# Optimization experiments

Hardware: AMD Instinct MI355X
Metric: run time of the kernel (lower is better)

## Reference

```python
import jax, jax.numpy as jnp
import numpy as np

NUM_ITER = 4
MIN_DISP = 1.0 / 100.0  # 1/max_depth
MAX_DISP = 1.0 / 0.1    # 1/min_depth


def _diag_embed(v):
    return v[..., :, None] * jnp.eye(v.shape[-1], dtype=v.dtype)


def _v2m(r):  # r: [B,3,1] -> antisymmetric [B,3,3]
    a1, a2, a3 = r[:, 0, 0], r[:, 1, 0], r[:, 2, 0]
    z = jnp.zeros_like(a1)
    return jnp.stack([z, -a3, a2, a3, z, -a1, -a2, a1, z], axis=-1).reshape(-1, 3, 3)


def _se3_pose(se3):  # se3: [B,6,1] -> [B,3,4]
    B = se3.shape[0]
    t, w = se3[:, 0:3], se3[:, 3:6]
    Nr = jnp.maximum(jnp.sqrt(jnp.sum(w * w, axis=1, keepdims=True)), 1e-12)  # [B,1,1]
    r = w / Nr
    I = jnp.eye(3, dtype=se3.dtype)[None]
    rx = _v2m(r)
    c, s = jnp.cos(Nr), jnp.sin(Nr)
    R = c * I + (1.0 - c) * jnp.matmul(r, jnp.transpose(r, (0, 2, 1))) + s * rx
    J = I + (Nr - s) / Nr * jnp.matmul(rx, rx) + (1.0 - c) / Nr * rx
    T = jnp.matmul(J, t)
    return jnp.concatenate([R, T], axis=2)


def _homogeneous(p34):
    B = p34.shape[0]
    ext = jnp.broadcast_to(jnp.array([[[0.0, 0.0, 0.0, 1.0]]], dtype=p34.dtype), (B, 1, 4))
    return jnp.concatenate([p34, ext], axis=1)


def _project_2d3d(points, depth, K_inv):  # [B,2,N],[B,1,N] -> [B,3,N]
    ones = jnp.ones_like(points[:, :1])
    xy3d = jnp.concatenate([points, ones], axis=1)
    return jnp.matmul(K_inv, xy3d) * depth


def _project_3d2d(p3d, K):
    q = jnp.matmul(K, p3d)
    return q[:, 0:2] / jnp.maximum(q[:, 2:3], 0.01)


def _reproject_error(p1, p2, disp, pose, K, K_inv):
    depth = 1.0 / jnp.maximum(disp, 0.01)
    p3d = _project_2d3d(p1, depth, K_inv)
    p3d_hat = jnp.matmul(pose[:, :3, :3], p3d) + pose[:, :3, 3:]
    return p2 - _project_3d2d(p3d_hat, K)


def _mean_on_mask(data, mask):  # reduce over last (point) dim, keepdims
    return jnp.sum(data * mask, axis=2, keepdims=True) / jnp.sum(mask, axis=2, keepdims=True)


def _jacobi_pose(p3d, K):  # -> [B,2,6,N]
    B, _, N = p3d.shape
    fx, fy = K[:, 0:1, 0:1], K[:, 1:2, 1:2]
    X, Y = p3d[:, 0:1], p3d[:, 1:2]
    Z = jnp.maximum(p3d[:, 2:3], 1e-12)
    iZ = 1.0 / Z
    iZ2 = iZ * iZ
    z = jnp.zeros_like(X)
    rows = [fx * iZ, z, -fx * X * iZ2, -fx * X * Y * iZ2, fx + fx * X * X * iZ2, -fx * Y * iZ,
            z, fy * iZ, -fy * Y * iZ2, -fy - fy * Y * Y * iZ2, fy * X * Y * iZ2, fy * X * iZ]
    return -jnp.concatenate(rows, axis=1).reshape(B, 2, 6, N)


def _jacobi_disp(p3d, pose, disps):  # -> [B,2,1,N]
    B, _, N = p3d.shape
    fx, fy = K0 = pose  # placeholder avoided below
    raise NotImplementedError


def _jacobi_disp_impl(p3d, pose, K, disps):  # -> [B,2,1,N]
    B, _, N = p3d.shape
    fx, fy = K[:, 0:1, 0:1], K[:, 1:2, 1:2]
    X, Y = p3d[:, 0:1], p3d[:, 1:2]
    Z = jnp.maximum(p3d[:, 2:3], 1e-12)
    iZ = 1.0 / Z
    iZ2 = iZ * iZ
    z = jnp.zeros_like(X)
    J1 = jnp.concatenate([fx * iZ, z, -fx * X * iZ2, z, fy * iZ, -fy * Y * iZ2], axis=1)
    J1 = jnp.transpose(J1.reshape(B, 2, 3, N), (0, 3, 1, 2))  # [B,N,2,3]
    T = pose[:, :3, 3:]  # [B,3,1]
    DD = -1.0 / disps    # [B,1,N]
    J2 = jnp.concatenate([DD * (X - T[:, 0:1]), (Y - T[:, 1:2]) * DD, (Z - T[:, 2:3]) * DD], axis=1)
    J2 = jnp.transpose(J2.reshape(B, 3, 1, N), (0, 3, 1, 2))  # [B,N,3,1]
    J = -jnp.matmul(J1, J2)                                   # [B,N,2,1]
    return jnp.transpose(J, (0, 2, 3, 1))                     # [B,2,1,N]


def _huber_w(err, mask, b=9.0):  # diag values of the [B,N,2,2] weight -> [B,N,2]
    B, _, N = err.shape
    en = jnp.sqrt(jnp.sum(err * err, axis=1, keepdims=True))          # [B,1,N]
    w = jnp.minimum(b / jnp.maximum(en, 1e-12), 1.0)
    w = jnp.sqrt(w) * mask                                            # [B,1,N]
    w = jnp.broadcast_to(jnp.transpose(w, (0, 2, 1)), (B, N, 2))
    return jax.lax.stop_gradient(w)


def _marginalization(Bm, E, C, V, W, L):
    Bsz, N = E.shape[0], E.shape[1]
    Bm = Bm + _diag_embed(jnp.diagonal(Bm, axis1=-2, axis2=-1)) * L   # L:[B,1,1]
    C = C + C * L.reshape(Bsz, 1, 1, 1)                               # C diag is itself (1x1)
    C_inv = 1.0 / jnp.maximum(C, 1.0)
    Bm = Bm + jnp.eye(6, dtype=Bm.dtype)
    Ev = E[..., 0]                 # [B,N,6]
    cinv = C_inv[:, :, 0, 0]       # [B,N]
    Wv = W[:, :, 0, 0]             # [B,N]
    Hsc = jnp.einsum('bn,bni,bnj->bij', cinv, Ev, Ev) / N
    bsc = (jnp.einsum('bn,bni,bn->bi', cinv, Ev, Wv) / N)[..., None]  # [B,6,1]
    invL = 1.0 / (1.0 + L)
    left = Bm - Hsc * invL
    right = V - bsc * invL
    s = 1.0 / jnp.sqrt(jnp.diagonal(left, axis1=-2, axis2=-1) + 10.0)  # [B,6]
    D = _diag_embed(s)
    H = D @ left @ D
    delta_pose = D @ jnp.linalg.solve(H, D @ right)                   # [B,6,1]
    p3d_sc = jnp.einsum('bni,bi->bn', Ev, delta_pose[:, :, 0]) * invL[:, 0, 0][:, None]
    delta_points = cinv * (Wv - p3d_sc)                               # [B,N]
    return delta_pose, delta_points


def _lm_step(pts_coord, pts_disp, pose, K, K_inv, mask, L):
    B, _, N = pts_coord.shape
    pts_depth = 1.0 / pts_disp
    p3d = _project_2d3d(pts_coord[:, 0:2], pts_depth, K_inv)
    p3d_hat = jnp.matmul(pose[:, :3, :3], p3d) + pose[:, :3, 3:]
    p2d_hat = _project_3d2d(p3d_hat, K)
    errors = pts_coord[:, 2:4] - p2d_hat                     # [B,2,N]
    J_pose = _jacobi_pose(p3d_hat, K)                        # [B,2,6,N]
    J_disp = _jacobi_disp_impl(p3d_hat, pose, K, pts_disp)   # [B,2,1,N]
    w = _huber_w(errors, mask)                               # [B,N,2]
    w2 = w * w
    Jp_T = jnp.transpose(J_pose, (0, 3, 2, 1))               # [B,N,6,2]
    Jd_T = jnp.transpose(J_disp, (0, 3, 2, 1))               # [B,N,1,2]
    Jp = jnp.transpose(J_pose, (0, 3, 1, 2))                 # [B,N,2,6]
    Jd = jnp.transpose(J_disp, (0, 3, 1, 2))                 # [B,N,2,1]
    Bm = jnp.einsum('bnik,bnkj->bij', Jp_T * w2[:, :, None, :], Jp) / N
    E = jnp.matmul(Jp_T * w2[:, :, None, :], Jd)             # [B,N,6,1]
    C = jnp.matmul(Jd_T * w2[:, :, None, :], Jd)             # [B,N,1,1]
    e = jnp.transpose(errors, (0, 2, 1))[..., None]          # [B,N,2,1]
    g_pose = -jnp.einsum('bnik,bnkj->bij', Jp_T * w[:, :, None, :], e) / N  # [B,6,1]
    g_disp = -jnp.matmul(Jd_T * w[:, :, None, :], e)         # [B,N,1,1]
    delta_pose, delta_points = _marginalization(Bm, E, C, g_pose, g_disp, L)
    return delta_pose, delta_points[:, None, :]              # [B,6,1], [B,1,N]


def reference(pts_coord, pts_disp, pose, K, K_inv, mask, L):
    for _ in range(NUM_ITER):
        dp, dd = _lm_step(pts_coord, pts_disp, pose, K, K_inv, mask, L)
        disp_new = jnp.clip(pts_disp + dd, MIN_DISP, MAX_DISP)
        pose_new = jnp.matmul(_homogeneous(_se3_pose(dp)), pose)
        e1 = _reproject_error(pts_coord[:, 0:2], pts_coord[:, 2:4], disp_new, pose_new, K, K_inv)
        e2 = _reproject_error(pts_coord[:, 0:2], pts_coord[:, 2:4], pts_disp, pose, K, K_inv)
        r1 = _mean_on_mask(jnp.linalg.norm(e1, axis=1, keepdims=True), mask)
        r2 = _mean_on_mask(jnp.linalg.norm(e2, axis=1, keepdims=True), mask)
        M = jax.lax.stop_gradient((r1 < r2).astype(pose.dtype))  # [B,1,1]
        pts_disp = jnp.where(M == 1, disp_new, pts_disp)
        pose = jnp.where(M == 1, pose_new, pose)
        L = jnp.clip(jnp.where(M == 1, L * 0.5, L * 5.0), 0.01, 1e6)
    return pose, pts_disp


def setup_inputs() -> dict:
    B, N = 8, 131072
    W, H = 640, 480
    key = jax.random.key(0)
    k = jax.random.split(key, 4)
    p1 = jax.random.uniform(k[0], (B, 2, N), dtype=jnp.float32) * jnp.array([W, H], jnp.float32).reshape(1, 2, 1)
    p2 = p1 + jax.random.normal(k[1], (B, 2, N), dtype=jnp.float32) * 2.0
    pts_coord = jnp.concatenate([p1, p2], axis=1)                      # [B,4,N]
    pts_disp = jax.random.uniform(k[2], (B, 1, N), dtype=jnp.float32, minval=0.05, maxval=2.0)
    pose = jnp.tile(jnp.eye(4, dtype=jnp.float32)[None], (B, 1, 1))
    pose = pose.at[:, :3, 3].set(jax.random.normal(k[3], (B, 3), dtype=jnp.float32) * 0.05)
    K = jnp.tile(jnp.array([[320.0, 0.0, 320.0], [0.0, 320.0, 240.0], [0.0, 0.0, 1.0]], jnp.float32)[None], (B, 1, 1))
    K_inv = jnp.linalg.inv(K)
    mask = jnp.ones((B, 1, N), jnp.float32)
    L = jnp.ones((B, 1, 1), jnp.float32) * 0.01
    return {'pts_coord': pts_coord, 'pts_disp': pts_disp, 'pose': pose, 'K': K, 'K_inv': K_inv, 'mask': mask, 'L': L}
```

## Files before the change

### kernel.cpp

```cpp
#include <hip/hip_runtime.h>
#include <math.h>


constexpr int TPB  = 256;
constexpr int BLKA = 64;
constexpr int NRED = 54;

__device__ __forceinline__ float wave_red(float v) {
#pragma unroll
  for (int m = 32; m; m >>= 1) v += __shfl_xor(v, m, 64);
  return v;
}

__device__ __forceinline__ float reproj_norm(
    float x1, float y1, float x2, float y2, float d,
    const float* P, const float* Kc, const float* Ki) {
  float depth = 1.0f / fmaxf(d, 0.01f);
  float pxx = (Ki[0]*x1 + Ki[1]*y1 + Ki[2]) * depth;
  float pyy = (Ki[3]*x1 + Ki[4]*y1 + Ki[5]) * depth;
  float pzz = (Ki[6]*x1 + Ki[7]*y1 + Ki[8]) * depth;
  float X = P[0]*pxx + P[1]*pyy + P[2]*pzz + P[3];
  float Y = P[4]*pxx + P[5]*pyy + P[6]*pzz + P[7];
  float Z = P[8]*pxx + P[9]*pyy + P[10]*pzz + P[11];
  float q0 = Kc[0]*X + Kc[1]*Y + Kc[2]*Z;
  float q1 = Kc[3]*X + Kc[4]*Y + Kc[5]*Z;
  float q2 = Kc[6]*X + Kc[7]*Y + Kc[8]*Z;
  float iZc = 1.0f / fmaxf(q2, 0.01f);
  float ex = x2 - q0*iZc, ey = y2 - q1*iZc;
  return sqrtf(ex*ex + ey*ey);
}

__device__ __forceinline__ float accept_M(const float* __restrict__ partB,
                                          int b) {
  float r1 = 0.0f, r2 = 0.0f, ms = 0.0f;
  for (int j = 0; j < BLKA; j++) {
    const float* p = partB + ((size_t)b*BLKA + j)*3;
    r1 += p[0]; r2 += p[1]; ms += p[2];
  }
  return ((r1/ms) < (r2/ms)) ? 1.0f : 0.0f;
}

__global__ __launch_bounds__(TPB) void kA(
    int it,
    const float* __restrict__ pts, const float* __restrict__ disp_src,
    const float* __restrict__ prop, const float* __restrict__ mask,
    const float* __restrict__ Kin, const float* __restrict__ Kiin,
    float* __restrict__ disp_cur,
    const float* __restrict__ pose0, const float* __restrict__ L0,
    const float* __restrict__ partB, const float* __restrict__ pose_new_ws,
    float* __restrict__ pose_slot_w, const float* __restrict__ pose_slot_r,
    float* __restrict__ L_slot_w, const float* __restrict__ L_slot_r,
    float* __restrict__ partA, int N) {
  const int b = blockIdx.y;

  __shared__ float sP[16];
  __shared__ float sMeta[2];
  if (threadIdx.x == 0) {
    float P[16], Lv, fs;
    if (it == 0) {
      for (int i = 0; i < 16; i++) P[i] = pose0[b*16+i];
      Lv = L0[b]; fs = 0.0f;
    } else {
      float M = accept_M(partB, b);
      fs = M;
      float Lp = L_slot_r[b];
      float Ln = (M != 0.0f) ? Lp*0.5f : Lp*5.0f;
      Lv = fminf(fmaxf(Ln, 0.01f), 1000000.0f);
      for (int i = 0; i < 16; i++)
        P[i] = (M != 0.0f) ? pose_new_ws[b*16+i] : pose_slot_r[b*16+i];
    }
    for (int i = 0; i < 16; i++) sP[i] = P[i];
    sMeta[0] = fs; sMeta[1] = Lv;
    if (blockIdx.x == 0) {
      for (int i = 0; i < 16; i++) pose_slot_w[b*16+i] = P[i];
      L_slot_w[b] = Lv;
    }
  }
  __syncthreads();

  float Kc[9], Ki[9], P[12];
#pragma unroll
  for (int i = 0; i < 9; i++) { Kc[i] = Kin[b*9+i]; Ki[i] = Kiin[b*9+i]; }
#pragma unroll
  for (int i = 0; i < 12; i++) P[i] = sP[i];
  const float onepL = 1.0f + sMeta[1];
  const float fsel = sMeta[0];
  const float fx = Kc[0], fy = Kc[4];

  float acc[NRED];
#pragma unroll
  for (int k = 0; k < NRED; k++) acc[k] = 0.0f;

  const size_t bN = (size_t)b * N;
  const float* px1 = pts + (size_t)b*4*N;
  const float* py1 = px1 + N;
  const float* px2 = px1 + 2*(size_t)N;
  const float* py2 = px1 + 3*(size_t)N;

  for (int n = blockIdx.x*TPB + threadIdx.x; n < N; n += gridDim.x*TPB) {
    float x1 = px1[n], y1 = py1[n], x2 = px2[n], y2 = py2[n];
    float d = disp_src[bN+n];
    if (fsel != 0.0f) d = prop[bN+n];
    disp_cur[bN+n] = d;
    float m = mask[bN+n];

    float depth = 1.0f / d;
    float pxx = (Ki[0]*x1 + Ki[1]*y1 + Ki[2]) * depth;
    float pyy = (Ki[3]*x1 + Ki[4]*y1 + Ki[5]) * depth;
    float pzz = (Ki[6]*x1 + Ki[7]*y1 + Ki[8]) * depth;
    float X = P[0]*pxx + P[1]*pyy + P[2]*pzz + P[3];
    float Y = P[4]*pxx + P[5]*pyy + P[6]*pzz + P[7];
    float Z = P[8]*pxx + P[9]*pyy + P[10]*pzz + P[11];
    float q0 = Kc[0]*X + Kc[1]*Y + Kc[2]*Z;
    float q1 = Kc[3]*X + Kc[4]*Y + Kc[5]*Z;
    float q2 = Kc[6]*X + Kc[7]*Y + Kc[8]*Z;
    float iZc = 1.0f / fmaxf(q2, 0.01f);
    float ex = x2 - q0*iZc;
    float ey = y2 - q1*iZc;
    float iZ = 1.0f / fmaxf(Z, 1e-12f);
    float iZ2 = iZ*iZ;

    float jp0[6], jp1[6];
    jp0[0] = -(fx*iZ);  jp0[1] = 0.0f;       jp0[2] = fx*X*iZ2;
    jp0[3] = fx*X*Y*iZ2; jp0[4] = -(fx + fx*X*X*iZ2); jp0[5] = fx*Y*iZ;
    jp1[0] = 0.0f;      jp1[1] = -(fy*iZ);   jp1[2] = fy*Y*iZ2;
    jp1[3] = fy + fy*Y*Y*iZ2; jp1[4] = -(fy*X*Y*iZ2); jp1[5] = -(fy*X*iZ);

    float DD = -depth;
    float dx = X - P[3], dy = Y - P[7], dz = Z - P[11];
    float jd0 = -((fx*iZ)*(DD*dx) - (fx*X*iZ2)*(DD*dz));
    float jd1 = -((fy*iZ)*(DD*dy) - (fy*Y*iZ2)*(DD*dz));

    float en = sqrtf(ex*ex + ey*ey);
    float wmin = fminf(9.0f / fmaxf(en, 1e-12f), 1.0f);
    float w  = sqrtf(wmin) * m;
    float w2 = w * w;

    float E[6];
#pragma unroll
    for (int k = 0; k < 6; k++) E[k] = w2*(jp0[k]*jd0 + jp1[k]*jd1);
    float C = w2*(jd0*jd0 + jd1*jd1);
    float cinv = 1.0f / fmaxf(C*onepL, 1.0f);
    float Wv = -w*(jd0*ex + jd1*ey);

    int idx = 0;
#pragma unroll
    for (int k = 0; k < 6; k++)
#pragma unroll
      for (int l = k; l < 6; l++) { acc[idx] += w2*(jp0[k]*jp0[l] + jp1[k]*jp1[l]); idx++; }
#pragma unroll
    for (int k = 0; k < 6; k++) acc[21+k] -= w*(jp0[k]*ex + jp1[k]*ey);
    idx = 27;
#pragma unroll
    for (int k = 0; k < 6; k++)
#pragma unroll
      for (int l = k; l < 6; l++) { acc[idx] += (cinv*E[k])*E[l]; idx++; }
#pragma unroll
    for (int k = 0; k < 6; k++) acc[48+k] += cinv*E[k]*Wv;
  }

  __shared__ float lds[TPB/64][NRED];
  const int lane = threadIdx.x & 63, wvi = threadIdx.x >> 6;
#pragma unroll
  for (int k = 0; k < NRED; k++) {
    float v = wave_red(acc[k]);
    if (lane == 0) lds[wvi][k] = v;
  }
  __syncthreads();
  if (threadIdx.x < NRED) {
    float s = 0.0f;
#pragma unroll
    for (int wq = 0; wq < TPB/64; wq++) s += lds[wq][threadIdx.x];
    partA[((size_t)b*gridDim.x + blockIdx.x)*NRED + threadIdx.x] = s;
  }
}

__global__ __launch_bounds__(TPB) void kB(
    const float* __restrict__ pts, const float* __restrict__ disp_cur,
    const float* __restrict__ mask,
    const float* __restrict__ Kin, const float* __restrict__ Kiin,
    const float* __restrict__ pose_slot, const float* __restrict__ L_slot,
    const float* __restrict__ partA,
    float* __restrict__ pose_new_ws,
    float* __restrict__ prop, float* __restrict__ partB, int N) {
  const int b = blockIdx.y;
  const float L = L_slot[b];

  __shared__ float S[NRED];
  __shared__ float sPn[16];
  __shared__ float sdp[6];
  if (threadIdx.x < NRED) {
    float s = 0.0f;
    for (int j = 0; j < BLKA; j++)
      s += partA[((size_t)b*BLKA + j)*NRED + threadIdx.x];
    S[threadIdx.x] = s;
  }
  __syncthreads();
  if (threadIdx.x == 0) {
    const float invN = 1.0f / (float)N;
    float Bm[6][6], Hs[6][6], g[6], bs[6];
    {
      int idx = 0;
      for (int k = 0; k < 6; k++)
        for (int l = k; l < 6; l++) { float v = S[idx++]*invN; Bm[k][l] = v; Bm[l][k] = v; }
      for (int k = 0; k < 6; k++) g[k] = S[21+k]*invN;
      idx = 27;
      for (int k = 0; k < 6; k++)
        for (int l = k; l < 6; l++) { float v = S[idx++]*invN; Hs[k][l] = v; Hs[l][k] = v; }
      for (int k = 0; k < 6; k++) bs[k] = S[48+k]*invN;
    }
    const float invL = 1.0f / (1.0f + L);
    float left[6][6], right[6];
    for (int k = 0; k < 6; k++) {
      for (int l = 0; l < 6; l++) {
        float v = Bm[k][l] - Hs[k][l]*invL;
        if (k == l) v += Bm[k][k]*L + 1.0f;
        left[k][l] = v;
      }
      right[k] = g[k] - bs[k]*invL;
    }
    float sv[6];
    for (int k = 0; k < 6; k++) sv[k] = 1.0f / sqrtf(left[k][k] + 10.0f);
    float H[6][7];
    for (int k = 0; k < 6; k++) {
      for (int l = 0; l < 6; l++) H[k][l] = sv[k]*left[k][l]*sv[l];
      H[k][6] = sv[k]*right[k];
    }
    for (int c = 0; c < 6; c++) {
      int piv = c; float mx = fabsf(H[c][c]);
      for (int r = c+1; r < 6; r++) { float a = fabsf(H[r][c]); if (a > mx) { mx = a; piv = r; } }
      if (piv != c)
        for (int cc2 = c; cc2 < 7; cc2++) { float tmp = H[c][cc2]; H[c][cc2] = H[piv][cc2]; H[piv][cc2] = tmp; }
      float ip = 1.0f / H[c][c];
      for (int r = c+1; r < 6; r++) {
        float f = H[r][c]*ip;
        for (int cc2 = c; cc2 < 7; cc2++) H[r][cc2] -= f*H[c][cc2];
      }
    }
    float x[6];
    for (int c = 5; c >= 0; c--) {
      float v = H[c][6];
      for (int cc2 = c+1; cc2 < 6; cc2++) v -= H[c][cc2]*x[cc2];
      x[c] = v / H[c][c];
    }
    float dp[6];
    for (int k = 0; k < 6; k++) { dp[k] = sv[k]*x[k]; sdp[k] = dp[k]; }

    float tx = dp[0], ty = dp[1], tz = dp[2];
    float wx = dp[3], wy = dp[4], wz = dp[5];
    float Nr = fmaxf(sqrtf(wx*wx + wy*wy + wz*wz), 1e-12f);
    float rx = wx/Nr, ry = wy/Nr, rz = wz/Nr;
    float c_ = cosf(Nr), sn = sinf(Nr);
    float omc = 1.0f - c_;
    float SK[3][3] = {{0.0f,-rz,ry},{rz,0.0f,-rx},{-ry,rx,0.0f}};
    float SK2[3][3];
    for (int i = 0; i < 3; i++)
      for (int j = 0; j < 3; j++) {
        float s2 = 0.0f;
        for (int k = 0; k < 3; k++) s2 += SK[i][k]*SK[k][j];
        SK2[i][j] = s2;
      }
    float rr[3] = {rx, ry, rz};
    float a = (Nr - sn)/Nr, bcoef = omc/Nr;
    float R3[3][3], Jm[3][3];
    for (int i = 0; i < 3; i++)
      for (int j = 0; j < 3; j++) {
        float eye = (i == j) ? 1.0f : 0.0f;
        R3[i][j] = c_*eye + omc*rr[i]*rr[j] + sn*SK[i][j];
        Jm[i][j] = eye + a*SK2[i][j] + bcoef*SK[i][j];
      }
    float T3[3];
    for (int i = 0; i < 3; i++) T3[i] = Jm[i][0]*tx + Jm[i][1]*ty + Jm[i][2]*tz;
    float Pc[16];
    for (int i = 0; i < 16; i++) Pc[i] = pose_slot[b*16+i];
    float Pn[16];
    for (int i = 0; i < 3; i++)
      for (int j = 0; j < 4; j++)
        Pn[i*4+j] = R3[i][0]*Pc[j] + R3[i][1]*Pc[4+j] + R3[i][2]*Pc[8+j] + T3[i]*Pc[12+j];
    for (int j = 0; j < 4; j++) Pn[12+j] = Pc[12+j];
    for (int i = 0; i < 16; i++) sPn[i] = Pn[i];
    if (blockIdx.x == 0)
      for (int i = 0; i < 16; i++) pose_new_ws[b*16+i] = Pn[i];
  }
  __syncthreads();

  float Kc[9], Ki[9], P[12], Pn[12], dp[6];
#pragma unroll
  for (int i = 0; i < 9; i++) { Kc[i] = Kin[b*9+i]; Ki[i] = Kiin[b*9+i]; }
#pragma unroll
  for (int i = 0; i < 12; i++) { P[i] = pose_slot[b*16+i]; Pn[i] = sPn[i]; }
#pragma unroll
  for (int i = 0; i < 6; i++) dp[i] = sdp[i];
  const float onepL = 1.0f + L;
  const float invL = 1.0f / onepL;
  const float fx = Kc[0], fy = Kc[4];

  float r1a = 0.0f, r2a = 0.0f, msa = 0.0f;
  const size_t bN = (size_t)b * N;
  const float* px1 = pts + (size_t)b*4*N;
  const float* py1 = px1 + N;
  const float* px2 = px1 + 2*(size_t)N;
  const float* py2 = px1 + 3*(size_t)N;

  for (int n = blockIdx.x*TPB + threadIdx.x; n < N; n += gridDim.x*TPB) {
    float x1 = px1[n], y1 = py1[n], x2 = px2[n], y2 = py2[n];
    float d = disp_cur[bN+n];
    float m = mask[bN+n];

    float depth = 1.0f / d;
    float pxx = (Ki[0]*x1 + Ki[1]*y1 + Ki[2]) * depth;
    float pyy = (Ki[3]*x1 + Ki[4]*y1 + Ki[5]) * depth;
    float pzz = (Ki[6]*x1 + Ki[7]*y1 + Ki[8]) * depth;
    float X = P[0]*pxx + P[1]*pyy + P[2]*pzz + P[3];
    float Y = P[4]*pxx + P[5]*pyy + P[6]*pzz + P[7];
    float Z = P[8]*pxx + P[9]*pyy + P[10]*pzz + P[11];
    float q0 = Kc[0]*X + Kc[1]*Y + Kc[2]*Z;
    float q1 = Kc[3]*X + Kc[4]*Y + Kc[5]*Z;
    float q2 = Kc[6]*X + Kc[7]*Y + Kc[8]*Z;
    float iZc = 1.0f / fmaxf(q2, 0.01f);
    float ex = x2 - q0*iZc;
    float ey = y2 - q1*iZc;
    float iZ = 1.0f / fmaxf(Z, 1e-12f);
    float iZ2 = iZ*iZ;

    float jp0[6], jp1[6];
    jp0[0] = -(fx*iZ);  jp0[1] = 0.0f;       jp0[2] = fx*X*iZ2;
    jp0[3] = fx*X*Y*iZ2; jp0[4] = -(fx + fx*X*X*iZ2); jp0[5] = fx*Y*iZ;
    jp1[0] = 0.0f;      jp1[1] = -(fy*iZ);   jp1[2] = fy*Y*iZ2;
    jp1[3] = fy + fy*Y*Y*iZ2; jp1[4] = -(fy*X*Y*iZ2); jp1[5] = -(fy*X*iZ);

    float DD = -depth;
    float dx = X - P[3], dy = Y - P[7], dz = Z - P[11];
    float jd0 = -((fx*iZ)*(DD*dx) - (fx*X*iZ2)*(DD*dz));
    float jd1 = -((fy*iZ)*(DD*dy) - (fy*Y*iZ2)*(DD*dz));

    float en = sqrtf(ex*ex + ey*ey);
    float wmin = fminf(9.0f / fmaxf(en, 1e-12f), 1.0f);
    float w  = sqrtf(wmin) * m;
    float w2 = w * w;

    float dotE = 0.0f;
#pragma unroll
    for (int k = 0; k < 6; k++) {
      float Ek = w2*(jp0[k]*jd0 + jp1[k]*jd1);
      dotE += Ek * dp[k];
    }
    float C = w2*(jd0*jd0 + jd1*jd1);
    float cinv = 1.0f / fmaxf(C*onepL, 1.0f);
    float Wv = -w*(jd0*ex + jd1*ey);

    float dnew = d + cinv*(Wv - dotE*invL);
    dnew = fminf(fmaxf(dnew, 0.01f), 10.0f);
    prop[bN+n] = dnew;

    float n1 = reproj_norm(x1, y1, x2, y2, dnew, Pn, Kc, Ki);
    float n2 = reproj_norm(x1, y1, x2, y2, d,    P,  Kc, Ki);
    r1a += n1*m; r2a += n2*m; msa += m;
  }

  __shared__ float lds[TPB/64][3];
  const int lane = threadIdx.x & 63, wvi = threadIdx.x >> 6;
  float v0 = wave_red(r1a), v1 = wave_red(r2a), v2 = wave_red(msa);
  if (lane == 0) { lds[wvi][0] = v0; lds[wvi][1] = v1; lds[wvi][2] = v2; }
  __syncthreads();
  if (threadIdx.x < 3) {
    float s = 0.0f;
#pragma unroll
    for (int wq = 0; wq < TPB/64; wq++) s += lds[wq][threadIdx.x];
    partB[((size_t)b*gridDim.x + blockIdx.x)*3 + threadIdx.x] = s;
  }
}

__global__ __launch_bounds__(TPB) void kF(
    const float* __restrict__ partB,
    const float* __restrict__ pose_slot, const float* __restrict__ pose_new_ws,
    const float* __restrict__ prop, float* __restrict__ dout, int N, int B) {
  const int b = blockIdx.y;
  __shared__ float sM[1];
  if (threadIdx.x == 0) sM[0] = accept_M(partB, b);
  __syncthreads();
  const float M = sM[0];

  if (blockIdx.x == 0 && threadIdx.x < 16) {
    float v = (M != 0.0f) ? pose_new_ws[b*16+threadIdx.x] : pose_slot[b*16+threadIdx.x];
    dout[b*16 + threadIdx.x] = v;
  }
  if (M == 0.0f) return;
  float* dd = dout + B*16;
  const size_t bN = (size_t)b * N;
  for (int n = blockIdx.x*TPB + threadIdx.x; n < N; n += gridDim.x*TPB)
    dd[bN+n] = prop[bN+n];
}

extern "C" void kernel_launch(void* const* d_in, const int* in_sizes, int n_in,
                              void* d_out, int out_size, void* d_ws, size_t ws_size,
                              hipStream_t stream) {
  const float* pts   = (const float*)d_in[0];
  const float* disp0 = (const float*)d_in[1];
  const float* pose0 = (const float*)d_in[2];
  const float* Kin   = (const float*)d_in[3];
  const float* Kiin  = (const float*)d_in[4];
  const float* mask  = (const float*)d_in[5];
  const float* L0    = (const float*)d_in[6];

  const int B = in_sizes[6];
  const int N = in_sizes[1] / B;
  const size_t BN = (size_t)B * N;

  float* out      = (float*)d_out;
  float* disp_cur = out + B*16;

  float* ws        = (float*)d_ws;
  float* prop      = ws;
  float* partA     = prop + BN;
  float* partB     = partA + (size_t)B*BLKA*NRED;
  float* pose_slots= partB + (size_t)B*BLKA*3;
  float* pose_new  = pose_slots + (size_t)2*B*16;
  float* L_slots   = pose_new + (size_t)B*16;

  dim3 gridBig(BLKA, B), blk(TPB);
  for (int it = 0; it < 4; ++it) {
    float* ps_w = pose_slots + (size_t)(it & 1) * B * 16;
    const float* ps_r = pose_slots + (size_t)((it + 1) & 1) * B * 16;
    float* Ls_w = L_slots + (size_t)(it & 1) * B;
    const float* Ls_r = L_slots + (size_t)((it + 1) & 1) * B;

    kA<<<gridBig, blk, 0, stream>>>(it, pts, (it == 0) ? disp0 : disp_cur, prop,
                                    mask, Kin, Kiin, disp_cur, pose0, L0,
                                    partB, pose_new, ps_w, ps_r, Ls_w, Ls_r,
                                    partA, N);
    kB<<<gridBig, blk, 0, stream>>>(pts, disp_cur, mask, Kin, Kiin,
                                    ps_w, Ls_w, partA, pose_new,
                                    prop, partB, N);
  }
  kF<<<gridBig, blk, 0, stream>>>(partB, pose_slots + (size_t)1*B*16, pose_new,
                                  prop, out, N, B);
}
```

Before: 285.4 us.

## Fuse all LM iterations into one cooperative kernel with register-resident disparities

Replaces the nine-kernel sequence (kA/kB per iteration plus kF) with a single cooperative launch of 256 blocks of 512 threads. Grid-wide syncs separate the reduction and solve phases, and each thread keeps its 8 disparities and proposals in registers across iterations, so the per-iteration global disp/prop round trips and launch overheads go away. The trade-offs are grid.sync latency, reliance on all blocks being co-resident, and higher register pressure from 54 accumulators plus 16 per-thread disparity values. If the cooperative launch fails, it falls back to the old multi-kernel path.

```diff
diff --git a/kernel.cpp b/kernel.cpp
--- a/kernel.cpp
+++ b/kernel.cpp
@@ -1,10 +1,18 @@
 #include <hip/hip_runtime.h>
+#include <hip/hip_cooperative_groups.h>
 #include <math.h>
 
+namespace cg = cooperative_groups;
+
+
+constexpr int NRED = 54;
+
+constexpr int CT   = 512;
+constexpr int CBPB = 32;
+constexpr int CPPT = 8;
 
 constexpr int TPB  = 256;
 constexpr int BLKA = 64;
-constexpr int NRED = 54;
 
 __device__ __forceinline__ float wave_red(float v) {
 #pragma unroll
@@ -30,8 +38,374 @@
   return sqrtf(ex*ex + ey*ey);
 }
 
-__device__ __forceinline__ float accept_M(const float* __restrict__ partB,
-                                          int b) {
+__device__ __forceinline__ void pointA(
+    float x1, float y1, float x2, float y2, float m, float d,
+    const float* P, const float* Kc, const float* Ki,
+    float fx, float fy, float onepL, float* acc) {
+  float depth = 1.0f / d;
+  float pxx = (Ki[0]*x1 + Ki[1]*y1 + Ki[2]) * depth;
+  float pyy = (Ki[3]*x1 + Ki[4]*y1 + Ki[5]) * depth;
+  float pzz = (Ki[6]*x1 + Ki[7]*y1 + Ki[8]) * depth;
+  float X = P[0]*pxx + P[1]*pyy + P[2]*pzz + P[3];
+  float Y = P[4]*pxx + P[5]*pyy + P[6]*pzz + P[7];
+  float Z = P[8]*pxx + P[9]*pyy + P[10]*pzz + P[11];
+  float q0 = Kc[0]*X + Kc[1]*Y + Kc[2]*Z;
+  float q1 = Kc[3]*X + Kc[4]*Y + Kc[5]*Z;
+  float q2 = Kc[6]*X + Kc[7]*Y + Kc[8]*Z;
+  float iZc = 1.0f / fmaxf(q2, 0.01f);
+  float ex = x2 - q0*iZc;
+  float ey = y2 - q1*iZc;
+  float iZ = 1.0f / fmaxf(Z, 1e-12f);
+  float iZ2 = iZ*iZ;
+
+  float jp0[6], jp1[6];
+  jp0[0] = -(fx*iZ);  jp0[1] = 0.0f;       jp0[2] = fx*X*iZ2;
+  jp0[3] = fx*X*Y*iZ2; jp0[4] = -(fx + fx*X*X*iZ2); jp0[5] = fx*Y*iZ;
+  jp1[0] = 0.0f;      jp1[1] = -(fy*iZ);   jp1[2] = fy*Y*iZ2;
+  jp1[3] = fy + fy*Y*Y*iZ2; jp1[4] = -(fy*X*Y*iZ2); jp1[5] = -(fy*X*iZ);
+
+  float DD = -depth;
+  float dx = X - P[3], dy = Y - P[7], dz = Z - P[11];
+  float jd0 = -((fx*iZ)*(DD*dx) - (fx*X*iZ2)*(DD*dz));
+  float jd1 = -((fy*iZ)*(DD*dy) - (fy*Y*iZ2)*(DD*dz));
+
+  float en = sqrtf(ex*ex + ey*ey);
+  float wmin = fminf(9.0f / fmaxf(en, 1e-12f), 1.0f);
+  float w  = sqrtf(wmin) * m;
+  float w2 = w * w;
+
+  float E[6];
+#pragma unroll
+  for (int k = 0; k < 6; k++) E[k] = w2*(jp0[k]*jd0 + jp1[k]*jd1);
+  float C = w2*(jd0*jd0 + jd1*jd1);
+  float cinv = 1.0f / fmaxf(C*onepL, 1.0f);
+  float Wv = -w*(jd0*ex + jd1*ey);
+
+  int idx = 0;
+#pragma unroll
+  for (int k = 0; k < 6; k++)
+#pragma unroll
+    for (int l = k; l < 6; l++) { acc[idx] += w2*(jp0[k]*jp0[l] + jp1[k]*jp1[l]); idx++; }
+#pragma unroll
+  for (int k = 0; k < 6; k++) acc[21+k] -= w*(jp0[k]*ex + jp1[k]*ey);
+  idx = 27;
+#pragma unroll
+  for (int k = 0; k < 6; k++)
+#pragma unroll
+    for (int l = k; l < 6; l++) { acc[idx] += (cinv*E[k])*E[l]; idx++; }
+#pragma unroll
+  for (int k = 0; k < 6; k++) acc[48+k] += cinv*E[k]*Wv;
+}
+
+__device__ __forceinline__ float pointB(
+    float x1, float y1, float x2, float y2, float m, float d,
+    const float* P, const float* Pn, const float* dp,
+    const float* Kc, const float* Ki,
+    float fx, float fy, float onepL, float invL,
+    float& r1a, float& r2a, float& msa) {
+  float depth = 1.0f / d;
+  float pxx = (Ki[0]*x1 + Ki[1]*y1 + Ki[2]) * depth;
+  float pyy = (Ki[3]*x1 + Ki[4]*y1 + Ki[5]) * depth;
+  float pzz = (Ki[6]*x1 + Ki[7]*y1 + Ki[8]) * depth;
+  float X = P[0]*pxx + P[1]*pyy + P[2]*pzz + P[3];
+  float Y = P[4]*pxx + P[5]*pyy + P[6]*pzz + P[7];
+  float Z = P[8]*pxx + P[9]*pyy + P[10]*pzz + P[11];
+  float q0 = Kc[0]*X + Kc[1]*Y + Kc[2]*Z;
+  float q1 = Kc[3]*X + Kc[4]*Y + Kc[5]*Z;
+  float q2 = Kc[6]*X + Kc[7]*Y + Kc[8]*Z;
+  float iZc = 1.0f / fmaxf(q2, 0.01f);
+  float ex = x2 - q0*iZc;
+  float ey = y2 - q1*iZc;
+  float iZ = 1.0f / fmaxf(Z, 1e-12f);
+  float iZ2 = iZ*iZ;
+
+  float jp0[6], jp1[6];
+  jp0[0] = -(fx*iZ);  jp0[1] = 0.0f;       jp0[2] = fx*X*iZ2;
+  jp0[3] = fx*X*Y*iZ2; jp0[4] = -(fx + fx*X*X*iZ2); jp0[5] = fx*Y*iZ;
+  jp1[0] = 0.0f;      jp1[1] = -(fy*iZ);   jp1[2] = fy*Y*iZ2;
+  jp1[3] = fy + fy*Y*Y*iZ2; jp1[4] = -(fy*X*Y*iZ2); jp1[5] = -(fy*X*iZ);
+
+  float DD = -depth;
+  float dx = X - P[3], dy = Y - P[7], dz = Z - P[11];
+  float jd0 = -((fx*iZ)*(DD*dx) - (fx*X*iZ2)*(DD*dz));
+  float jd1 = -((fy*iZ)*(DD*dy) - (fy*Y*iZ2)*(DD*dz));
+
+  float en = sqrtf(ex*ex + ey*ey);
+  float wmin = fminf(9.0f / fmaxf(en, 1e-12f), 1.0f);
+  float w  = sqrtf(wmin) * m;
+  float w2 = w * w;
+
+  float dotE = 0.0f;
+#pragma unroll
+  for (int k = 0; k < 6; k++) {
+    float Ek = w2*(jp0[k]*jd0 + jp1[k]*jd1);
+    dotE += Ek * dp[k];
+  }
+  float C = w2*(jd0*jd0 + jd1*jd1);
+  float cinv = 1.0f / fmaxf(C*onepL, 1.0f);
+  float Wv = -w*(jd0*ex + jd1*ey);
+
+  float dnew = d + cinv*(Wv - dotE*invL);
+  dnew = fminf(fmaxf(dnew, 0.01f), 10.0f);
+
+  float n1 = reproj_norm(x1, y1, x2, y2, dnew, Pn, Kc, Ki);
+  float n2 = reproj_norm(x1, y1, x2, y2, d,    P,  Kc, Ki);
+  r1a += n1*m; r2a += n2*m; msa += m;
+  return dnew;
+}
+
+__device__ void solve_scalar(const float* S, float L, const float* Pc_in,
+                             float invN, float* dp_out, float* Pn_out) {
+  float Bm[6][6], Hs[6][6], g[6], bs[6];
+  {
+    int idx = 0;
+    for (int k = 0; k < 6; k++)
+      for (int l = k; l < 6; l++) { float v = S[idx++]*invN; Bm[k][l] = v; Bm[l][k] = v; }
+    for (int k = 0; k < 6; k++) g[k] = S[21+k]*invN;
+    idx = 27;
+    for (int k = 0; k < 6; k++)
+      for (int l = k; l < 6; l++) { float v = S[idx++]*invN; Hs[k][l] = v; Hs[l][k] = v; }
+    for (int k = 0; k < 6; k++) bs[k] = S[48+k]*invN;
+  }
+  const float invL = 1.0f / (1.0f + L);
+  float left[6][6], right[6];
+  for (int k = 0; k < 6; k++) {
+    for (int l = 0; l < 6; l++) {
+      float v = Bm[k][l] - Hs[k][l]*invL;
+      if (k == l) v += Bm[k][k]*L + 1.0f;
+      left[k][l] = v;
+    }
+    right[k] = g[k] - bs[k]*invL;
+  }
+  float sv[6];
+  for (int k = 0; k < 6; k++) sv[k] = 1.0f / sqrtf(left[k][k] + 10.0f);
+  float H[6][7];
+  for (int k = 0; k < 6; k++) {
+    for (int l = 0; l < 6; l++) H[k][l] = sv[k]*left[k][l]*sv[l];
+    H[k][6] = sv[k]*right[k];
+  }
+  for (int c = 0; c < 6; c++) {
+    int piv = c; float mx = fabsf(H[c][c]);
+    for (int r = c+1; r < 6; r++) { float a = fabsf(H[r][c]); if (a > mx) { mx = a; piv = r; } }
+    if (piv != c)
+      for (int cc2 = c; cc2 < 7; cc2++) { float tmp = H[c][cc2]; H[c][cc2] = H[piv][cc2]; H[piv][cc2] = tmp; }
+    float ip = 1.0f / H[c][c];
+    for (int r = c+1; r < 6; r++) {
+      float f = H[r][c]*ip;
+      for (int cc2 = c; cc2 < 7; cc2++) H[r][cc2] -= f*H[c][cc2];
+    }
+  }
+  float x[6];
+  for (int c = 5; c >= 0; c--) {
+    float v = H[c][6];
+    for (int cc2 = c+1; cc2 < 6; cc2++) v -= H[c][cc2]*x[cc2];
+    x[c] = v / H[c][c];
+  }
+  float dp[6];
+  for (int k = 0; k < 6; k++) { dp[k] = sv[k]*x[k]; dp_out[k] = dp[k]; }
+
+  float tx = dp[0], ty = dp[1], tz = dp[2];
+  float wx = dp[3], wy = dp[4], wz = dp[5];
+  float Nr = fmaxf(sqrtf(wx*wx + wy*wy + wz*wz), 1e-12f);
+  float rx = wx/Nr, ry = wy/Nr, rz = wz/Nr;
+  float c_ = cosf(Nr), sn = sinf(Nr);
+  float omc = 1.0f - c_;
+  float SK[3][3] = {{0.0f,-rz,ry},{rz,0.0f,-rx},{-ry,rx,0.0f}};
+  float SK2[3][3];
+  for (int i = 0; i < 3; i++)
+    for (int j2 = 0; j2 < 3; j2++) {
+      float s2 = 0.0f;
+      for (int k = 0; k < 3; k++) s2 += SK[i][k]*SK[k][j2];
+      SK2[i][j2] = s2;
+    }
+  float rr[3] = {rx, ry, rz};
+  float a = (Nr - sn)/Nr, bcoef = omc/Nr;
+  float R3[3][3], Jm[3][3];
+  for (int i = 0; i < 3; i++)
+    for (int j2 = 0; j2 < 3; j2++) {
+      float eye = (i == j2) ? 1.0f : 0.0f;
+      R3[i][j2] = c_*eye + omc*rr[i]*rr[j2] + sn*SK[i][j2];
+      Jm[i][j2] = eye + a*SK2[i][j2] + bcoef*SK[i][j2];
+    }
+  float T3[3];
+  for (int i = 0; i < 3; i++) T3[i] = Jm[i][0]*tx + Jm[i][1]*ty + Jm[i][2]*tz;
+  for (int i = 0; i < 3; i++)
+    for (int j2 = 0; j2 < 4; j2++)
+      Pn_out[i*4+j2] = R3[i][0]*Pc_in[j2] + R3[i][1]*Pc_in[4+j2] + R3[i][2]*Pc_in[8+j2] + T3[i]*Pc_in[12+j2];
+  for (int j2 = 0; j2 < 4; j2++) Pn_out[12+j2] = Pc_in[12+j2];
+}
+
+__global__ __launch_bounds__(CT, 2) void kCoop(
+    const float* __restrict__ pts, const float* __restrict__ disp0,
+    const float* __restrict__ mask, const float* __restrict__ Kin,
+    const float* __restrict__ Kiin, const float* __restrict__ pose0,
+    const float* __restrict__ L0,
+    float* __restrict__ partA, float* __restrict__ partB,
+    float* __restrict__ dout, int N, int B) {
+  cg::grid_group grid = cg::this_grid();
+  const int b   = blockIdx.x / CBPB;
+  const int bx  = blockIdx.x % CBPB;
+  const int tid = threadIdx.x;
+  const int lane = tid & 63, wvi = tid >> 6;
+
+  __shared__ float sP[16];
+  __shared__ float sPn[16];
+  __shared__ float sdp[6];
+  __shared__ float sS[NRED];
+  __shared__ float sMeta[2];
+  __shared__ float lds54[CT/64][NRED];
+  __shared__ float lds3[CT/64][3];
+
+  float Kc[9], Ki[9];
+#pragma unroll
+  for (int i = 0; i < 9; i++) { Kc[i] = Kin[b*9+i]; Ki[i] = Kiin[b*9+i]; }
+  const float fx = Kc[0], fy = Kc[4];
+
+  if (tid == 0) {
+#pragma unroll
+    for (int i = 0; i < 16; i++) sP[i] = pose0[b*16+i];
+    sMeta[0] = 0.0f; sMeta[1] = L0[b];
+  }
+  __syncthreads();
+
+  const size_t bN = (size_t)b * N;
+  const float* px1 = pts + (size_t)b*4*N;
+  const float* py1 = px1 + N;
+  const float* px2 = px1 + 2*(size_t)N;
+  const float* py2 = px1 + 3*(size_t)N;
+  const int n0 = bx*CT + tid;
+  constexpr int STRIDE = CBPB*CT;
+
+  float d[CPPT], dn[CPPT];
+#pragma unroll
+  for (int j = 0; j < CPPT; j++) {
+    int n = n0 + j*STRIDE;
+    d[j]  = (n < N) ? disp0[bN+n] : 1.0f;
+    dn[j] = d[j];
+  }
+
+  for (int it = 0; it < 4; ++it) {
+    if (it > 0) {
+      if (tid == 0) {
+        float r1 = 0.0f, r2 = 0.0f, ms = 0.0f;
+        for (int j = 0; j < CBPB; j++) {
+          const float* p = partB + ((size_t)b*CBPB + j)*3;
+          r1 += p[0]; r2 += p[1]; ms += p[2];
+        }
+        float M = ((r1/ms) < (r2/ms)) ? 1.0f : 0.0f;
+        sMeta[0] = M;
+        float Lp = sMeta[1];
+        float Ln = (M != 0.0f) ? Lp*0.5f : Lp*5.0f;
+        sMeta[1] = fminf(fmaxf(Ln, 0.01f), 1000000.0f);
+        if (M != 0.0f)
+          for (int i = 0; i < 16; i++) sP[i] = sPn[i];
+      }
+      __syncthreads();
+      if (sMeta[0] != 0.0f) {
+#pragma unroll
+        for (int j = 0; j < CPPT; j++) d[j] = dn[j];
+      }
+    }
+    const float onepL = 1.0f + sMeta[1];
+    float P[12];
+#pragma unroll
+    for (int i = 0; i < 12; i++) P[i] = sP[i];
+
+    float acc[NRED];
+#pragma unroll
+    for (int k = 0; k < NRED; k++) acc[k] = 0.0f;
+#pragma unroll
+    for (int j = 0; j < CPPT; j++) {
+      int n = n0 + j*STRIDE;
+      float x1 = 0.0f, y1 = 0.0f, x2 = 0.0f, y2 = 0.0f, m = 0.0f;
+      if (n < N) { x1 = px1[n]; y1 = py1[n]; x2 = px2[n]; y2 = py2[n]; m = mask[bN+n]; }
+      pointA(x1, y1, x2, y2, m, d[j], P, Kc, Ki, fx, fy, onepL, acc);
+    }
+#pragma unroll
+    for (int k = 0; k < NRED; k++) {
+      float v = wave_red(acc[k]);
+      if (lane == 0) lds54[wvi][k] = v;
+    }
+    __syncthreads();
+    if (tid < NRED) {
+      float s = 0.0f;
+#pragma unroll
+      for (int wq = 0; wq < CT/64; wq++) s += lds54[wq][tid];
+      partA[((size_t)b*CBPB + bx)*NRED + tid] = s;
+    }
+    grid.sync();
+
+    if (tid < NRED) {
+      float s = 0.0f;
+      for (int j = 0; j < CBPB; j++)
+        s += partA[((size_t)b*CBPB + j)*NRED + tid];
+      sS[tid] = s;
+    }
+    __syncthreads();
+    if (tid == 0) {
+      float dpl[6], Pnl[16], Pcl[16], Sl[NRED];
+      for (int i = 0; i < NRED; i++) Sl[i] = sS[i];
+      for (int i = 0; i < 16; i++) Pcl[i] = sP[i];
+      solve_scalar(Sl, sMeta[1], Pcl, 1.0f / (float)N, dpl, Pnl);
+      for (int i = 0; i < 6; i++) sdp[i] = dpl[i];
+      for (int i = 0; i < 16; i++) sPn[i] = Pnl[i];
+    }
+    __syncthreads();
+
+    float Pn[12], dp[6];
+#pragma unroll
+    for (int i = 0; i < 12; i++) Pn[i] = sPn[i];
+#pragma unroll
+    for (int i = 0; i < 6; i++) dp[i] = sdp[i];
+    const float invL = 1.0f / onepL;
+
+    float r1a = 0.0f, r2a = 0.0f, msa = 0.0f;
+#pragma unroll
+    for (int j = 0; j < CPPT; j++) {
+      int n = n0 + j*STRIDE;
+      float x1 = 0.0f, y1 = 0.0f, x2 = 0.0f, y2 = 0.0f, m = 0.0f;
+      if (n < N) { x1 = px1[n]; y1 = py1[n]; x2 = px2[n]; y2 = py2[n]; m = mask[bN+n]; }
+      dn[j] = pointB(x1, y1, x2, y2, m, d[j], P, Pn, dp, Kc, Ki,
+                     fx, fy, onepL, invL, r1a, r2a, msa);
+    }
+    {
+      float v0 = wave_red(r1a), v1 = wave_red(r2a), v2 = wave_red(msa);
+      if (lane == 0) { lds3[wvi][0] = v0; lds3[wvi][1] = v1; lds3[wvi][2] = v2; }
+    }
+    __syncthreads();
+    if (tid < 3) {
+      float s = 0.0f;
+#pragma unroll
+      for (int wq = 0; wq < CT/64; wq++) s += lds3[wq][tid];
+      partB[((size_t)b*CBPB + bx)*3 + tid] = s;
+    }
+    grid.sync();
+  }
+
+  if (tid == 0) {
+    float r1 = 0.0f, r2 = 0.0f, ms = 0.0f;
+    for (int j = 0; j < CBPB; j++) {
+      const float* p = partB + ((size_t)b*CBPB + j)*3;
+      r1 += p[0]; r2 += p[1]; ms += p[2];
+    }
+    float M = ((r1/ms) < (r2/ms)) ? 1.0f : 0.0f;
+    sMeta[0] = M;
+    if (M != 0.0f)
+      for (int i = 0; i < 16; i++) sP[i] = sPn[i];
+  }
+  __syncthreads();
+  const float Mf = sMeta[0];
+
+  if (bx == 0 && tid < 16) dout[b*16 + tid] = sP[tid];
+  float* dd = dout + B*16;
+#pragma unroll
+  for (int j = 0; j < CPPT; j++) {
+    int n = n0 + j*STRIDE;
+    if (n < N) dd[bN+n] = (Mf != 0.0f) ? dn[j] : d[j];
+  }
+}
+
+__device__ __forceinline__ float accept_M_fb(const float* __restrict__ partB, int b) {
   float r1 = 0.0f, r2 = 0.0f, ms = 0.0f;
   for (int j = 0; j < BLKA; j++) {
     const float* p = partB + ((size_t)b*BLKA + j)*3;
@@ -40,7 +414,7 @@
   return ((r1/ms) < (r2/ms)) ? 1.0f : 0.0f;
 }
 
-__global__ __launch_bounds__(TPB) void kA(
+__global__ __launch_bounds__(TPB) void fb_kA(
     int it,
     const float* __restrict__ pts, const float* __restrict__ disp_src,
     const float* __restrict__ prop, const float* __restrict__ mask,
@@ -61,7 +435,7 @@
       for (int i = 0; i < 16; i++) P[i] = pose0[b*16+i];
       Lv = L0[b]; fs = 0.0f;
     } else {
-      float M = accept_M(partB, b);
+      float M = accept_M_fb(partB, b);
       fs = M;
       float Lp = L_slot_r[b];
       float Ln = (M != 0.0f) ? Lp*0.5f : Lp*5.0f;
@@ -103,60 +477,7 @@
     if (fsel != 0.0f) d = prop[bN+n];
     disp_cur[bN+n] = d;
     float m = mask[bN+n];
-
-    float depth = 1.0f / d;
-    float pxx = (Ki[0]*x1 + Ki[1]*y1 + Ki[2]) * depth;
-    float pyy = (Ki[3]*x1 + Ki[4]*y1 + Ki[5]) * depth;
-    float pzz = (Ki[6]*x1 + Ki[7]*y1 + Ki[8]) * depth;
-    float X = P[0]*pxx + P[1]*pyy + P[2]*pzz + P[3];
-    float Y = P[4]*pxx + P[5]*pyy + P[6]*pzz + P[7];
-    float Z = P[8]*pxx + P[9]*pyy + P[10]*pzz + P[11];
-    float q0 = Kc[0]*X + Kc[1]*Y + Kc[2]*Z;
-    float q1 = Kc[3]*X + Kc[4]*Y + Kc[5]*Z;
-    float q2 = Kc[6]*X + Kc[7]*Y + Kc[8]*Z;
-    float iZc = 1.0f / fmaxf(q2, 0.01f);
-    float ex = x2 - q0*iZc;
-    float ey = y2 - q1*iZc;
-    float iZ = 1.0f / fmaxf(Z, 1e-12f);
-    float iZ2 = iZ*iZ;
-
-    float jp0[6], jp1[6];
-    jp0[0] = -(fx*iZ);  jp0[1] = 0.0f;       jp0[2] = fx*X*iZ2;
-    jp0[3] = fx*X*Y*iZ2; jp0[4] = -(fx + fx*X*X*iZ2); jp0[5] = fx*Y*iZ;
-    jp1[0] = 0.0f;      jp1[1] = -(fy*iZ);   jp1[2] = fy*Y*iZ2;
-    jp1[3] = fy + fy*Y*Y*iZ2; jp1[4] = -(fy*X*Y*iZ2); jp1[5] = -(fy*X*iZ);
-
-    float DD = -depth;
-    float dx = X - P[3], dy = Y - P[7], dz = Z - P[11];
-    float jd0 = -((fx*iZ)*(DD*dx) - (fx*X*iZ2)*(DD*dz));
-    float jd1 = -((fy*iZ)*(DD*dy) - (fy*Y*iZ2)*(DD*dz));
-
-    float en = sqrtf(ex*ex + ey*ey);
-    float wmin = fminf(9.0f / fmaxf(en, 1e-12f), 1.0f);
-    float w  = sqrtf(wmin) * m;
-    float w2 = w * w;
-
-    float E[6];
-#pragma unroll
-    for (int k = 0; k < 6; k++) E[k] = w2*(jp0[k]*jd0 + jp1[k]*jd1);
-    float C = w2*(jd0*jd0 + jd1*jd1);
-    float cinv = 1.0f / fmaxf(C*onepL, 1.0f);
-    float Wv = -w*(jd0*ex + jd1*ey);
-
-    int idx = 0;
-#pragma unroll
-    for (int k = 0; k < 6; k++)
-#pragma unroll
-      for (int l = k; l < 6; l++) { acc[idx] += w2*(jp0[k]*jp0[l] + jp1[k]*jp1[l]); idx++; }
-#pragma unroll
-    for (int k = 0; k < 6; k++) acc[21+k] -= w*(jp0[k]*ex + jp1[k]*ey);
-    idx = 27;
-#pragma unroll
-    for (int k = 0; k < 6; k++)
-#pragma unroll
-      for (int l = k; l < 6; l++) { acc[idx] += (cinv*E[k])*E[l]; idx++; }
-#pragma unroll
-    for (int k = 0; k < 6; k++) acc[48+k] += cinv*E[k]*Wv;
+    pointA(x1, y1, x2, y2, m, d, P, Kc, Ki, fx, fy, onepL, acc);
   }
 
   __shared__ float lds[TPB/64][NRED];
@@ -175,7 +496,7 @@
   }
 }
 
-__global__ __launch_bounds__(TPB) void kB(
+__global__ __launch_bounds__(TPB) void fb_kB(
     const float* __restrict__ pts, const float* __restrict__ disp_cur,
     const float* __restrict__ mask,
     const float* __restrict__ Kin, const float* __restrict__ Kiin,
@@ -197,90 +518,14 @@
   }
   __syncthreads();
   if (threadIdx.x == 0) {
-    const float invN = 1.0f / (float)N;
-    float Bm[6][6], Hs[6][6], g[6], bs[6];
-    {
-      int idx = 0;
-      for (int k = 0; k < 6; k++)
-        for (int l = k; l < 6; l++) { float v = S[idx++]*invN; Bm[k][l] = v; Bm[l][k] = v; }
-      for (int k = 0; k < 6; k++) g[k] = S[21+k]*invN;
-      idx = 27;
-      for (int k = 0; k < 6; k++)
-        for (int l = k; l < 6; l++) { float v = S[idx++]*invN; Hs[k][l] = v; Hs[l][k] = v; }
-      for (int k = 0; k < 6; k++) bs[k] = S[48+k]*invN;
-    }
-    const float invL = 1.0f / (1.0f + L);
-    float left[6][6], right[6];
-    for (int k = 0; k < 6; k++) {
-      for (int l = 0; l < 6; l++) {
-        float v = Bm[k][l] - Hs[k][l]*invL;
-        if (k == l) v += Bm[k][k]*L + 1.0f;
-        left[k][l] = v;
-      }
-      right[k] = g[k] - bs[k]*invL;
-    }
-    float sv[6];
-    for (int k = 0; k < 6; k++) sv[k] = 1.0f / sqrtf(left[k][k] + 10.0f);
-    float H[6][7];
-    for (int k = 0; k < 6; k++) {
-      for (int l = 0; l < 6; l++) H[k][l] = sv[k]*left[k][l]*sv[l];
-      H[k][6] = sv[k]*right[k];
-    }
-    for (int c = 0; c < 6; c++) {
-      int piv = c; float mx = fabsf(H[c][c]);
-      for (int r = c+1; r < 6; r++) { float a = fabsf(H[r][c]); if (a > mx) { mx = a; piv = r; } }
-      if (piv != c)
-        for (int cc2 = c; cc2 < 7; cc2++) { float tmp = H[c][cc2]; H[c][cc2] = H[piv][cc2]; H[piv][cc2] = tmp; }
-      float ip = 1.0f / H[c][c];
-      for (int r = c+1; r < 6; r++) {
-        float f = H[r][c]*ip;
-        for (int cc2 = c; cc2 < 7; cc2++) H[r][cc2] -= f*H[c][cc2];
-      }
-    }
-    float x[6];
-    for (int c = 5; c >= 0; c--) {
-      float v = H[c][6];
-      for (int cc2 = c+1; cc2 < 6; cc2++) v -= H[c][cc2]*x[cc2];
-      x[c] = v / H[c][c];
-    }
-    float dp[6];
-    for (int k = 0; k < 6; k++) { dp[k] = sv[k]*x[k]; sdp[k] = dp[k]; }
-
-    float tx = dp[0], ty = dp[1], tz = dp[2];
-    float wx = dp[3], wy = dp[4], wz = dp[5];
-    float Nr = fmaxf(sqrtf(wx*wx + wy*wy + wz*wz), 1e-12f);
-    float rx = wx/Nr, ry = wy/Nr, rz = wz/Nr;
-    float c_ = cosf(Nr), sn = sinf(Nr);
-    float omc = 1.0f - c_;
-    float SK[3][3] = {{0.0f,-rz,ry},{rz,0.0f,-rx},{-ry,rx,0.0f}};
-    float SK2[3][3];
-    for (int i = 0; i < 3; i++)
-      for (int j = 0; j < 3; j++) {
-        float s2 = 0.0f;
-        for (int k = 0; k < 3; k++) s2 += SK[i][k]*SK[k][j];
-        SK2[i][j] = s2;
-      }
-    float rr[3] = {rx, ry, rz};
-    float a = (Nr - sn)/Nr, bcoef = omc/Nr;
-    float R3[3][3], Jm[3][3];
-    for (int i = 0; i < 3; i++)
-      for (int j = 0; j < 3; j++) {
-        float eye = (i == j) ? 1.0f : 0.0f;
-        R3[i][j] = c_*eye + omc*rr[i]*rr[j] + sn*SK[i][j];
-        Jm[i][j] = eye + a*SK2[i][j] + bcoef*SK[i][j];
-      }
-    float T3[3];
-    for (int i = 0; i < 3; i++) T3[i] = Jm[i][0]*tx + Jm[i][1]*ty + Jm[i][2]*tz;
-    float Pc[16];
-    for (int i = 0; i < 16; i++) Pc[i] = pose_slot[b*16+i];
-    float Pn[16];
-    for (int i = 0; i < 3; i++)
-      for (int j = 0; j < 4; j++)
-        Pn[i*4+j] = R3[i][0]*Pc[j] + R3[i][1]*Pc[4+j] + R3[i][2]*Pc[8+j] + T3[i]*Pc[12+j];
-    for (int j = 0; j < 4; j++) Pn[12+j] = Pc[12+j];
-    for (int i = 0; i < 16; i++) sPn[i] = Pn[i];
+    float dpl[6], Pnl[16], Pcl[16], Sl[NRED];
+    for (int i = 0; i < NRED; i++) Sl[i] = S[i];
+    for (int i = 0; i < 16; i++) Pcl[i] = pose_slot[b*16+i];
+    solve_scalar(Sl, L, Pcl, 1.0f / (float)N, dpl, Pnl);
+    for (int i = 0; i < 6; i++) sdp[i] = dpl[i];
+    for (int i = 0; i < 16; i++) sPn[i] = Pnl[i];
     if (blockIdx.x == 0)
-      for (int i = 0; i < 16; i++) pose_new_ws[b*16+i] = Pn[i];
+      for (int i = 0; i < 16; i++) pose_new_ws[b*16+i] = Pnl[i];
   }
   __syncthreads();
 
@@ -306,56 +551,9 @@
     float x1 = px1[n], y1 = py1[n], x2 = px2[n], y2 = py2[n];
     float d = disp_cur[bN+n];
     float m = mask[bN+n];
-
-    float depth = 1.0f / d;
-    float pxx = (Ki[0]*x1 + Ki[1]*y1 + Ki[2]) * depth;
-    float pyy = (Ki[3]*x1 + Ki[4]*y1 + Ki[5]) * depth;
-    float pzz = (Ki[6]*x1 + Ki[7]*y1 + Ki[8]) * depth;
-    float X = P[0]*pxx + P[1]*pyy + P[2]*pzz + P[3];
-    float Y = P[4]*pxx + P[5]*pyy + P[6]*pzz + P[7];
-    float Z = P[8]*pxx + P[9]*pyy + P[10]*pzz + P[11];
-    float q0 = Kc[0]*X + Kc[1]*Y + Kc[2]*Z;
-    float q1 = Kc[3]*X + Kc[4]*Y + Kc[5]*Z;
-    float q2 = Kc[6]*X + Kc[7]*Y + Kc[8]*Z;
-    float iZc = 1.0f / fmaxf(q2, 0.01f);
-    float ex = x2 - q0*iZc;
-    float ey = y2 - q1*iZc;
-    float iZ = 1.0f / fmaxf(Z, 1e-12f);
-    float iZ2 = iZ*iZ;
-
-    float jp0[6], jp1[6];
-    jp0[0] = -(fx*iZ);  jp0[1] = 0.0f;       jp0[2] = fx*X*iZ2;
-    jp0[3] = fx*X*Y*iZ2; jp0[4] = -(fx + fx*X*X*iZ2); jp0[5] = fx*Y*iZ;
-    jp1[0] = 0.0f;      jp1[1] = -(fy*iZ);   jp1[2] = fy*Y*iZ2;
-    jp1[3] = fy + fy*Y*Y*iZ2; jp1[4] = -(fy*X*Y*iZ2); jp1[5] = -(fy*X*iZ);
-
-    float DD = -depth;
-    float dx = X - P[3], dy = Y - P[7], dz = Z - P[11];
-    float jd0 = -((fx*iZ)*(DD*dx) - (fx*X*iZ2)*(DD*dz));
-    float jd1 = -((fy*iZ)*(DD*dy) - (fy*Y*iZ2)*(DD*dz));
-
-    float en = sqrtf(ex*ex + ey*ey);
-    float wmin = fminf(9.0f / fmaxf(en, 1e-12f), 1.0f);
-    float w  = sqrtf(wmin) * m;
-    float w2 = w * w;
-
-    float dotE = 0.0f;
-#pragma unroll
-    for (int k = 0; k < 6; k++) {
-      float Ek = w2*(jp0[k]*jd0 + jp1[k]*jd1);
-      dotE += Ek * dp[k];
-    }
-    float C = w2*(jd0*jd0 + jd1*jd1);
-    float cinv = 1.0f / fmaxf(C*onepL, 1.0f);
-    float Wv = -w*(jd0*ex + jd1*ey);
-
-    float dnew = d + cinv*(Wv - dotE*invL);
-    dnew = fminf(fmaxf(dnew, 0.01f), 10.0f);
+    float dnew = pointB(x1, y1, x2, y2, m, d, P, Pn, dp, Kc, Ki,
+                        fx, fy, onepL, invL, r1a, r2a, msa);
     prop[bN+n] = dnew;
-
-    float n1 = reproj_norm(x1, y1, x2, y2, dnew, Pn, Kc, Ki);
-    float n2 = reproj_norm(x1, y1, x2, y2, d,    P,  Kc, Ki);
-    r1a += n1*m; r2a += n2*m; msa += m;
   }
 
   __shared__ float lds[TPB/64][3];
@@ -371,13 +569,13 @@
   }
 }
 
-__global__ __launch_bounds__(TPB) void kF(
+__global__ __launch_bounds__(TPB) void fb_kF(
     const float* __restrict__ partB,
     const float* __restrict__ pose_slot, const float* __restrict__ pose_new_ws,
     const float* __restrict__ prop, float* __restrict__ dout, int N, int B) {
   const int b = blockIdx.y;
   __shared__ float sM[1];
-  if (threadIdx.x == 0) sM[0] = accept_M(partB, b);
+  if (threadIdx.x == 0) sM[0] = accept_M_fb(partB, b);
   __syncthreads();
   const float M = sM[0];
 
@@ -412,11 +610,22 @@
 
   float* ws        = (float*)d_ws;
   float* prop      = ws;
-  float* partA     = prop + BN;
-  float* partB     = partA + (size_t)B*BLKA*NRED;
-  float* pose_slots= partB + (size_t)B*BLKA*3;
+  float* partA_fb  = prop + BN;
+  float* partB_fb  = partA_fb + (size_t)B*BLKA*NRED;
+  float* pose_slots= partB_fb + (size_t)B*BLKA*3;
   float* pose_new  = pose_slots + (size_t)2*B*16;
   float* L_slots   = pose_new + (size_t)B*16;
+  float* partA_cp  = L_slots + (size_t)2*B;
+  float* partB_cp  = partA_cp + (size_t)B*CBPB*NRED;
+
+  void* args[] = {(void*)&pts, (void*)&disp0, (void*)&mask, (void*)&Kin,
+                  (void*)&Kiin, (void*)&pose0, (void*)&L0,
+                  (void*)&partA_cp, (void*)&partB_cp, (void*)&out,
+                  (void*)&N, (void*)&B};
+  hipError_t ce = hipLaunchCooperativeKernel((void*)kCoop, dim3(B*CBPB),
+                                             dim3(CT), args, 0, stream);
+  if (ce == hipSuccess) return;
+  (void)hipGetLastError();
 
   dim3 gridBig(BLKA, B), blk(TPB);
   for (int it = 0; it < 4; ++it) {
@@ -425,14 +634,14 @@
     float* Ls_w = L_slots + (size_t)(it & 1) * B;
     const float* Ls_r = L_slots + (size_t)((it + 1) & 1) * B;
 
-    kA<<<gridBig, blk, 0, stream>>>(it, pts, (it == 0) ? disp0 : disp_cur, prop,
-                                    mask, Kin, Kiin, disp_cur, pose0, L0,
-                                    partB, pose_new, ps_w, ps_r, Ls_w, Ls_r,
-                                    partA, N);
-    kB<<<gridBig, blk, 0, stream>>>(pts, disp_cur, mask, Kin, Kiin,
-                                    ps_w, Ls_w, partA, pose_new,
-                                    prop, partB, N);
-  }
-  kF<<<gridBig, blk, 0, stream>>>(partB, pose_slots + (size_t)1*B*16, pose_new,
-                                  prop, out, N, B);
-}
+    fb_kA<<<gridBig, blk, 0, stream>>>(it, pts, (it == 0) ? disp0 : disp_cur, prop,
+                                       mask, Kin, Kiin, disp_cur, pose0, L0,
+                                       partB_fb, pose_new, ps_w, ps_r, Ls_w, Ls_r,
+                                       partA_fb, N);
+    fb_kB<<<gridBig, blk, 0, stream>>>(pts, disp_cur, mask, Kin, Kiin,
+                                       ps_w, Ls_w, partA_fb, pose_new,
+                                       prop, partB_fb, N);
+  }
+  fb_kF<<<gridBig, blk, 0, stream>>>(partB_fb, pose_slots + (size_t)1*B*16,
+                                     pose_new, prop, out, N, B);
+}
```

Measured after the change: 519.6 us. 1.82x slower.
